# Kernel optimization log

Hardware: AMD Instinct MI355X
Metric: run time of the kernel (lower is better)

## Reference

```python
import jax, jax.numpy as jnp
import numpy as np

EPS_ENERGY = 1e-05
EPS_NORM = 1e-05
DN = ('NWC', 'WIO', 'NWC')  # conv1d dimension numbers: (B,L,C) x (K,Cin,Cout)


def setup_inputs() -> dict:
    key = jax.random.key(0)
    k1, k2 = jax.random.split(key)
    B, L, C = 16, 32768, 21
    K, F = 9, 128
    inputs = jax.random.normal(k1, (B, L, C), dtype=jnp.float32)
    kernel = jax.random.normal(k2, (K, C, F), dtype=jnp.float32)
    # UnitNorm constraint over axes [0, 1] (per output filter)
    kernel = kernel / jnp.sqrt(jnp.sum(kernel * kernel, axis=(0, 1), keepdims=True))
    scale = jnp.full((1, 1, 1), 10.0, dtype=jnp.float32)  # initial_scale
    bias = jnp.zeros((F,), dtype=jnp.float32)
    return {"inputs": inputs, "kernel": kernel, "scale": scale, "bias": bias}


def reference(inputs, kernel, scale, bias):
    # dot: (B, L-K+1, F)
    dot = jax.lax.conv_general_dilated(
        inputs, kernel, window_strides=(1,), padding='VALID',
        dimension_numbers=DN)
    # patch energy: sliding sum of squares over window and ALL input channels.
    # Original convolves sq_inputs with an all-ones (K, C, F) kernel, producing
    # the identical value in every filter channel; we compute it once with a
    # (K, C, 1) ones kernel and broadcast -- same math, less traffic.
    K, C, _ = kernel.shape
    ones_k = jnp.ones((K, C, 1), dtype=inputs.dtype)
    patch_energy = jax.lax.conv_general_dilated(
        inputs * inputs, ones_k, window_strides=(1,), padding='VALID',
        dimension_numbers=DN)  # (B, Lout, 1)
    patch_norms = jnp.sqrt(patch_energy + EPS_ENERGY)
    return scale * (dot / (patch_norms + EPS_NORM)) + bias
```

## Files before the change

### kernel.cpp

```cpp
#include <hip/hip_runtime.h>
#include <hip/hip_bf16.h>
#include <math.h>

typedef __bf16 bf16x8 __attribute__((ext_vector_type(8)));
typedef float  f32x4  __attribute__((ext_vector_type(4)));
typedef unsigned short u16x8 __attribute__((ext_vector_type(8)));

#define B_      16
#define LIN_    32768
#define LOUT_   32760
#define CIN_    21
#define CPAD_   24
#define KT_     9
#define F_      128
#define KSTEPS_ 7
#define TILE_L_ 128
#define ROWS_   136
#define ROWSA_  138
#define NTILE_  256
#define LPAD_   32768
#define IB_ROWS_ 1024
#define IB_PER_B 32
#define WP_OFF_FLOATS_ (B_ * LPAD_)
#define WP_SHORTS_ (4 * KSTEPS_ * 2 * 4 * 16 * 8)

__device__ __forceinline__ unsigned short f2bf(float f) {
  unsigned u = __float_as_uint(f);
  u += 0x7FFFu + ((u >> 16) & 1u);
  return (unsigned short)(u >> 16);
}

__global__ __launch_bounds__(256)
void ckn1d_prep(const float* __restrict__ X, const float* __restrict__ W,
                const float* __restrict__ scale_p, float* __restrict__ ws)
{
  const int tid = threadIdx.x;
  const int bid = blockIdx.x;

  if (bid < B_ * IB_PER_B) {
    __shared__ float rowsq[IB_ROWS_ + 8];
    const int b    = bid >> 5;
    const int base = (bid & (IB_PER_B - 1)) * IB_ROWS_;
    const float scale = scale_p[0];
    const float* Xb = X + (size_t)b * LIN_ * CIN_;

    for (int r = tid; r < IB_ROWS_ + 8; r += 256) {
      int row = base + r;
      float s = 0.f;
      if (row < LIN_) {
        const float* xr = Xb + (size_t)row * CIN_;
        #pragma unroll
        for (int c = 0; c < CIN_; ++c) { float x = xr[c]; s += x * x; }
      }
      rowsq[r] = s;
    }
    __syncthreads();

    const int l0 = tid * 4;
    float e0 = 0.f;
    #pragma unroll
    for (int t = 0; t < KT_; ++t) e0 += rowsq[l0 + t];
    float e1 = e0 - rowsq[l0]     + rowsq[l0 + KT_];
    float e2 = e1 - rowsq[l0 + 1] + rowsq[l0 + 1 + KT_];
    float e3 = e2 - rowsq[l0 + 2] + rowsq[l0 + 2 + KT_];
    f32x4 iv;
    iv[0] = scale / (sqrtf(e0 + 1e-5f) + 1e-5f);
    iv[1] = scale / (sqrtf(e1 + 1e-5f) + 1e-5f);
    iv[2] = scale / (sqrtf(e2 + 1e-5f) + 1e-5f);
    iv[3] = scale / (sqrtf(e3 + 1e-5f) + 1e-5f);
    float* invp = ws + (size_t)b * LPAD_ + base + l0;
    if (base + l0 + 3 < LOUT_) {
      *(f32x4*)invp = iv;
    } else {
      #pragma unroll
      for (int u = 0; u < 4; ++u)
        if (base + l0 + u < LOUT_) invp[u] = iv[u];
    }
  } else {
    const int wv = bid - B_ * IB_PER_B;
    unsigned short* Wp = (unsigned short*)(ws + WP_OFF_FLOATS_);
    for (int idx = tid; idx < KSTEPS_ * 2 * 4 * 16; idx += 256) {
      int t   = idx >> 7;
      int rem = idx & 127;
      int nf  = rem >> 6;
      int q   = (rem >> 4) & 3;
      int la  = rem & 15;
      u16x8 v;
      #pragma unroll
      for (int j = 0; j < 8; ++j) {
        int r = t * 32 + q * 8 + j;
        int k = r / CPAD_;
        int c = r - k * CPAD_;
        float w = 0.f;
        if (c < CIN_ && k < KT_) w = W[(k * CIN_ + c) * F_ + wv * 32 + nf * 16 + la];
        v[j] = f2bf(w);
      }
      *(u16x8*)&Wp[(size_t)((((wv * KSTEPS_ + t) * 2 + nf) * 4 + q) * 16 + la) * 8] = v;
    }
  }
}

__global__ __launch_bounds__(256, 4)
void ckn1d_main(const float* __restrict__ X, const float* __restrict__ ws,
                const float* __restrict__ bias_p, float* __restrict__ Y)
{
  __shared__ __align__(16) unsigned short tileA[ROWSA_ * CPAD_];

  const int tid  = threadIdx.x;
  const int wv   = tid >> 6;
  const int lane = tid & 63;
  const int la   = lane & 15;
  const int q    = lane >> 4;

  const int bx   = blockIdx.x;
  const int b    = bx >> 8;
  const int tile = bx & (NTILE_ - 1);
  const int l0t  = tile * TILE_L_;

  const int f0 = wv * 32 + la;
  const float bias0 = bias_p[f0];
  const float bias1 = bias_p[f0 + 16];

  const float* __restrict__ Xb   = X + (size_t)b * LIN_ * CIN_;
  const float* __restrict__ invb = ws + (size_t)b * LPAD_ + l0t;
  const unsigned short* __restrict__ Wp = (const unsigned short*)(ws + WP_OFF_FLOATS_);
  float* __restrict__ Yb = Y + (size_t)b * LOUT_ * F_;

  for (int i = tid; i < ROWSA_ * 3; i += 256) {
    int r = i / 3;
    tileA[r * CPAD_ + CIN_ + (i - r * 3)] = 0;
  }
  for (int i = tid; i < 2 * CIN_; i += 256) {
    int r = ROWS_ + i / CIN_;
    tileA[r * CPAD_ + (i % CIN_)] = 0;
  }
  {
    const float4* src4 = (const float4*)(Xb + (size_t)l0t * CIN_);
    const int n4v = (min(ROWS_, LIN_ - l0t) * CIN_) >> 2;
    for (int i4 = tid; i4 < (ROWS_ * CIN_) / 4; i4 += 256) {
      float4 v;
      if (i4 < n4v) v = src4[i4];
      else          v = make_float4(0.f, 0.f, 0.f, 0.f);
      int base = i4 * 4;
      #pragma unroll
      for (int e = 0; e < 4; ++e) {
        int idx = base + e;
        int r = idx / CIN_;
        int c = idx - r * CIN_;
        float x = (e == 0) ? v.x : (e == 1) ? v.y : (e == 2) ? v.z : v.w;
        tileA[r * CPAD_ + c] = f2bf(x);
      }
    }
  }

  u16x8 bw[KSTEPS_][2];
  #pragma unroll
  for (int t = 0; t < KSTEPS_; ++t)
    #pragma unroll
    for (int nf = 0; nf < 2; ++nf)
      bw[t][nf] = *(const u16x8*)&Wp[(size_t)((((wv * KSTEPS_ + t) * 2 + nf) * 4 + q) * 16 + la) * 8];

  __syncthreads();

  const f32x4 fzero = {0.f, 0.f, 0.f, 0.f};
  const bool full = (l0t + TILE_L_) <= LOUT_;

  #pragma unroll 1
  for (int mf = 0; mf < TILE_L_ / 16; ++mf) {
    const unsigned short* arow = &tileA[(mf * 16 + la) * CPAD_ + q * 8];
    f32x4 a0 = fzero, a1 = fzero;
    #pragma unroll
    for (int t = 0; t < KSTEPS_; ++t) {
      bf16x8 a = *(const bf16x8*)&arow[t * 32];
      a0 = __builtin_amdgcn_mfma_f32_16x16x32_bf16(
          a, __builtin_bit_cast(bf16x8, bw[t][0]), a0, 0, 0, 0);
      a1 = __builtin_amdgcn_mfma_f32_16x16x32_bf16(
          a, __builtin_bit_cast(bf16x8, bw[t][1]), a1, 0, 0, 0);
    }
    const int lrow0 = mf * 16 + q * 4;
    const f32x4 iv4 = *(const f32x4*)&invb[lrow0];
    float* yo = Yb + (size_t)(l0t + lrow0) * F_ + f0;
    if (full) {
      #pragma unroll
      for (int rg = 0; rg < 4; ++rg) {
        float iv = iv4[rg];
        yo[(size_t)rg * F_]      = a0[rg] * iv + bias0;
        yo[(size_t)rg * F_ + 16] = a1[rg] * iv + bias1;
      }
    } else {
      #pragma unroll
      for (int rg = 0; rg < 4; ++rg) {
        float iv = iv4[rg];
        if (l0t + lrow0 + rg < LOUT_) {
          yo[(size_t)rg * F_]      = a0[rg] * iv + bias0;
          yo[(size_t)rg * F_ + 16] = a1[rg] * iv + bias1;
        }
      }
    }
  }
}

extern "C" void kernel_launch(void* const* d_in, const int* in_sizes, int n_in,
                              void* d_out, int out_size, void* d_ws, size_t ws_size,
                              hipStream_t stream) {
  const float* X  = (const float*)d_in[0];
  const float* W  = (const float*)d_in[1];
  const float* S  = (const float*)d_in[2];
  const float* Bi = (const float*)d_in[3];
  float* Y  = (float*)d_out;
  float* ws = (float*)d_ws;

  dim3 gprep(B_ * IB_PER_B + 4), block(256);
  ckn1d_prep<<<gprep, block, 0, stream>>>(X, W, S, ws);

  dim3 gmain(B_ * NTILE_);
  ckn1d_main<<<gmain, block, 0, stream>>>(X, ws, Bi, Y);
}
```

Baseline: 76.75 us.

## Fuse patch-energy normalization into main conv kernel using LDS row sums

Moves the per-position sliding sum of squares and inverse-norm computation out of the prep kernel and into the main kernel. Row energies are accumulated with LDS atomics while the input tile is staged, and the inverse norms are kept in shared memory. This removes a second full read of the input, plus the global write and read of the inverse-norm array. In exchange it adds LDS atomics and two extra barriers per block, and the prep kernel now only packs the weights.

Result: slower. 102.2 us (+33.2%).

```diff
diff --git a/kernel.cpp b/kernel.cpp
--- a/kernel.cpp
+++ b/kernel.cpp
@@ -18,10 +18,6 @@
 #define ROWS_   136
 #define ROWSA_  138
 #define NTILE_  256
-#define LPAD_   32768
-#define IB_ROWS_ 1024
-#define IB_PER_B 32
-#define WP_OFF_FLOATS_ (B_ * LPAD_)
 #define WP_SHORTS_ (4 * KSTEPS_ * 2 * 4 * 16 * 8)
 
 __device__ __forceinline__ unsigned short f2bf(float f) {
@@ -30,81 +26,45 @@
   return (unsigned short)(u >> 16);
 }
 
+__device__ __forceinline__ void bar_lds() {
+  asm volatile("s_waitcnt lgkmcnt(0)" ::: "memory");
+  __builtin_amdgcn_s_barrier();
+}
+
 __global__ __launch_bounds__(256)
-void ckn1d_prep(const float* __restrict__ X, const float* __restrict__ W,
-                const float* __restrict__ scale_p, float* __restrict__ ws)
+void ckn1d_prep(const float* __restrict__ W, float* __restrict__ ws)
 {
   const int tid = threadIdx.x;
-  const int bid = blockIdx.x;
-
-  if (bid < B_ * IB_PER_B) {
-    __shared__ float rowsq[IB_ROWS_ + 8];
-    const int b    = bid >> 5;
-    const int base = (bid & (IB_PER_B - 1)) * IB_ROWS_;
-    const float scale = scale_p[0];
-    const float* Xb = X + (size_t)b * LIN_ * CIN_;
-
-    for (int r = tid; r < IB_ROWS_ + 8; r += 256) {
-      int row = base + r;
-      float s = 0.f;
-      if (row < LIN_) {
-        const float* xr = Xb + (size_t)row * CIN_;
-        #pragma unroll
-        for (int c = 0; c < CIN_; ++c) { float x = xr[c]; s += x * x; }
-      }
-      rowsq[r] = s;
+  const int wv  = blockIdx.x;
+  unsigned short* Wp = (unsigned short*)ws;
+  for (int idx = tid; idx < KSTEPS_ * 2 * 4 * 16; idx += 256) {
+    int t   = idx >> 7;
+    int rem = idx & 127;
+    int nf  = rem >> 6;
+    int q   = (rem >> 4) & 3;
+    int la  = rem & 15;
+    u16x8 v;
+    #pragma unroll
+    for (int j = 0; j < 8; ++j) {
+      int r = t * 32 + q * 8 + j;
+      int k = r / CPAD_;
+      int c = r - k * CPAD_;
+      float w = 0.f;
+      if (c < CIN_ && k < KT_) w = W[(k * CIN_ + c) * F_ + wv * 32 + nf * 16 + la];
+      v[j] = f2bf(w);
     }
-    __syncthreads();
-
-    const int l0 = tid * 4;
-    float e0 = 0.f;
-    #pragma unroll
-    for (int t = 0; t < KT_; ++t) e0 += rowsq[l0 + t];
-    float e1 = e0 - rowsq[l0]     + rowsq[l0 + KT_];
-    float e2 = e1 - rowsq[l0 + 1] + rowsq[l0 + 1 + KT_];
-    float e3 = e2 - rowsq[l0 + 2] + rowsq[l0 + 2 + KT_];
-    f32x4 iv;
-    iv[0] = scale / (sqrtf(e0 + 1e-5f) + 1e-5f);
-    iv[1] = scale / (sqrtf(e1 + 1e-5f) + 1e-5f);
-    iv[2] = scale / (sqrtf(e2 + 1e-5f) + 1e-5f);
-    iv[3] = scale / (sqrtf(e3 + 1e-5f) + 1e-5f);
-    float* invp = ws + (size_t)b * LPAD_ + base + l0;
-    if (base + l0 + 3 < LOUT_) {
-      *(f32x4*)invp = iv;
-    } else {
-      #pragma unroll
-      for (int u = 0; u < 4; ++u)
-        if (base + l0 + u < LOUT_) invp[u] = iv[u];
-    }
-  } else {
-    const int wv = bid - B_ * IB_PER_B;
-    unsigned short* Wp = (unsigned short*)(ws + WP_OFF_FLOATS_);
-    for (int idx = tid; idx < KSTEPS_ * 2 * 4 * 16; idx += 256) {
-      int t   = idx >> 7;
-      int rem = idx & 127;
-      int nf  = rem >> 6;
-      int q   = (rem >> 4) & 3;
-      int la  = rem & 15;
-      u16x8 v;
-      #pragma unroll
-      for (int j = 0; j < 8; ++j) {
-        int r = t * 32 + q * 8 + j;
-        int k = r / CPAD_;
-        int c = r - k * CPAD_;
-        float w = 0.f;
-        if (c < CIN_ && k < KT_) w = W[(k * CIN_ + c) * F_ + wv * 32 + nf * 16 + la];
-        v[j] = f2bf(w);
-      }
-      *(u16x8*)&Wp[(size_t)((((wv * KSTEPS_ + t) * 2 + nf) * 4 + q) * 16 + la) * 8] = v;
-    }
+    *(u16x8*)&Wp[(size_t)((((wv * KSTEPS_ + t) * 2 + nf) * 4 + q) * 16 + la) * 8] = v;
   }
 }
 
 __global__ __launch_bounds__(256, 4)
 void ckn1d_main(const float* __restrict__ X, const float* __restrict__ ws,
-                const float* __restrict__ bias_p, float* __restrict__ Y)
+                const float* __restrict__ scale_p, const float* __restrict__ bias_p,
+                float* __restrict__ Y)
 {
   __shared__ __align__(16) unsigned short tileA[ROWSA_ * CPAD_];
+  __shared__ float rowsq[ROWS_];
+  __shared__ __align__(16) float inv_s[TILE_L_];
 
   const int tid  = threadIdx.x;
   const int wv   = tid >> 6;
@@ -118,14 +78,15 @@
   const int l0t  = tile * TILE_L_;
 
   const int f0 = wv * 32 + la;
+  const float scale = scale_p[0];
   const float bias0 = bias_p[f0];
   const float bias1 = bias_p[f0 + 16];
 
-  const float* __restrict__ Xb   = X + (size_t)b * LIN_ * CIN_;
-  const float* __restrict__ invb = ws + (size_t)b * LPAD_ + l0t;
-  const unsigned short* __restrict__ Wp = (const unsigned short*)(ws + WP_OFF_FLOATS_);
+  const float* __restrict__ Xb = X + (size_t)b * LIN_ * CIN_;
+  const unsigned short* __restrict__ Wp = (const unsigned short*)ws;
   float* __restrict__ Yb = Y + (size_t)b * LOUT_ * F_;
 
+  if (tid < ROWS_) rowsq[tid] = 0.f;
   for (int i = tid; i < ROWSA_ * 3; i += 256) {
     int r = i / 3;
     tileA[r * CPAD_ + CIN_ + (i - r * 3)] = 0;
@@ -133,24 +94,6 @@
   for (int i = tid; i < 2 * CIN_; i += 256) {
     int r = ROWS_ + i / CIN_;
     tileA[r * CPAD_ + (i % CIN_)] = 0;
-  }
-  {
-    const float4* src4 = (const float4*)(Xb + (size_t)l0t * CIN_);
-    const int n4v = (min(ROWS_, LIN_ - l0t) * CIN_) >> 2;
-    for (int i4 = tid; i4 < (ROWS_ * CIN_) / 4; i4 += 256) {
-      float4 v;
-      if (i4 < n4v) v = src4[i4];
-      else          v = make_float4(0.f, 0.f, 0.f, 0.f);
-      int base = i4 * 4;
-      #pragma unroll
-      for (int e = 0; e < 4; ++e) {
-        int idx = base + e;
-        int r = idx / CIN_;
-        int c = idx - r * CIN_;
-        float x = (e == 0) ? v.x : (e == 1) ? v.y : (e == 2) ? v.z : v.w;
-        tileA[r * CPAD_ + c] = f2bf(x);
-      }
-    }
   }
 
   u16x8 bw[KSTEPS_][2];
@@ -160,7 +103,40 @@
     for (int nf = 0; nf < 2; ++nf)
       bw[t][nf] = *(const u16x8*)&Wp[(size_t)((((wv * KSTEPS_ + t) * 2 + nf) * 4 + q) * 16 + la) * 8];
 
-  __syncthreads();
+  bar_lds();
+
+  {
+    const float4* src4 = (const float4*)(Xb + (size_t)l0t * CIN_);
+    const int n4v = (min(ROWS_, LIN_ - l0t) * CIN_) >> 2;
+    for (int i4 = tid; i4 < (ROWS_ * CIN_) / 4; i4 += 256) {
+      float4 v;
+      if (i4 < n4v) v = src4[i4];
+      else          v = make_float4(0.f, 0.f, 0.f, 0.f);
+      int base = i4 * 4;
+      int r0 = base / CIN_;
+      float s0 = 0.f, s1 = 0.f;
+      #pragma unroll
+      for (int e = 0; e < 4; ++e) {
+        int idx = base + e;
+        int r = idx / CIN_;
+        int c = idx - r * CIN_;
+        float x = (e == 0) ? v.x : (e == 1) ? v.y : (e == 2) ? v.z : v.w;
+        tileA[r * CPAD_ + c] = f2bf(x);
+        if (r == r0) s0 += x * x; else s1 += x * x;
+      }
+      atomicAdd(&rowsq[r0], s0);
+      if (s1 != 0.f && r0 + 1 < ROWS_) atomicAdd(&rowsq[r0 + 1], s1);
+    }
+  }
+  bar_lds();
+
+  if (tid < TILE_L_) {
+    float e = 0.f;
+    #pragma unroll
+    for (int t = 0; t < KT_; ++t) e += rowsq[tid + t];
+    inv_s[tid] = scale / (sqrtf(e + 1e-5f) + 1e-5f);
+  }
+  bar_lds();
 
   const f32x4 fzero = {0.f, 0.f, 0.f, 0.f};
   const bool full = (l0t + TILE_L_) <= LOUT_;
@@ -178,7 +154,7 @@
           a, __builtin_bit_cast(bf16x8, bw[t][1]), a1, 0, 0, 0);
     }
     const int lrow0 = mf * 16 + q * 4;
-    const f32x4 iv4 = *(const f32x4*)&invb[lrow0];
+    const f32x4 iv4 = *(const f32x4*)&inv_s[lrow0];
     float* yo = Yb + (size_t)(l0t + lrow0) * F_ + f0;
     if (full) {
       #pragma unroll
@@ -210,9 +186,6 @@
   float* Y  = (float*)d_out;
   float* ws = (float*)d_ws;
 
-  dim3 gprep(B_ * IB_PER_B + 4), block(256);
-  ckn1d_prep<<<gprep, block, 0, stream>>>(X, W, S, ws);
-
-  dim3 gmain(B_ * NTILE_);
-  ckn1d_main<<<gmain, block, 0, stream>>>(X, ws, Bi, Y);
+  ckn1d_prep<<<dim3(4), dim3(256), 0, stream>>>(W, ws);
+  ckn1d_main<<<dim3(B_ * NTILE_), dim3(256), 0, stream>>>(X, ws, S, Bi, Y);
 }
```

## Stage output tiles in LDS for coalesced float4 global stores

Applied to the files above, without the earlier changes.

Outputs are now written first to a shared-memory buffer of 32 rows by 128 filters, after two MFMA m-fragments per pass. All 256 threads then write that buffer to global memory as contiguous float4 rows. This replaces the scattered scalar stores, which are strided by 16 floats across lanes, and is meant to improve write coalescing on an output-bandwidth-bound kernel. It adds about 17KB of LDS, which may reduce occupancy, plus extra barriers per pass.

After: 68.96 us, median of 2. 10.1% less time.

```diff
diff --git a/kernel.cpp b/kernel.cpp
--- a/kernel.cpp
+++ b/kernel.cpp
@@ -19,15 +19,20 @@
 #define ROWSA_  138
 #define NTILE_  256
 #define LPAD_   32768
+#define OBST_   136
 #define IB_ROWS_ 1024
 #define IB_PER_B 32
 #define WP_OFF_FLOATS_ (B_ * LPAD_)
-#define WP_SHORTS_ (4 * KSTEPS_ * 2 * 4 * 16 * 8)
 
 __device__ __forceinline__ unsigned short f2bf(float f) {
   unsigned u = __float_as_uint(f);
   u += 0x7FFFu + ((u >> 16) & 1u);
   return (unsigned short)(u >> 16);
+}
+
+__device__ __forceinline__ void bar_lds() {
+  asm volatile("s_waitcnt lgkmcnt(0)" ::: "memory");
+  __builtin_amdgcn_s_barrier();
 }
 
 __global__ __launch_bounds__(256)
@@ -105,6 +110,7 @@
                 const float* __restrict__ bias_p, float* __restrict__ Y)
 {
   __shared__ __align__(16) unsigned short tileA[ROWSA_ * CPAD_];
+  __shared__ __align__(16) float outbuf[32 * OBST_];
 
   const int tid  = threadIdx.x;
   const int wv   = tid >> 6;
@@ -160,40 +166,54 @@
     for (int nf = 0; nf < 2; ++nf)
       bw[t][nf] = *(const u16x8*)&Wp[(size_t)((((wv * KSTEPS_ + t) * 2 + nf) * 4 + q) * 16 + la) * 8];
 
-  __syncthreads();
+  bar_lds();
 
   const f32x4 fzero = {0.f, 0.f, 0.f, 0.f};
-  const bool full = (l0t + TILE_L_) <= LOUT_;
 
   #pragma unroll 1
-  for (int mf = 0; mf < TILE_L_ / 16; ++mf) {
-    const unsigned short* arow = &tileA[(mf * 16 + la) * CPAD_ + q * 8];
-    f32x4 a0 = fzero, a1 = fzero;
-    #pragma unroll
-    for (int t = 0; t < KSTEPS_; ++t) {
-      bf16x8 a = *(const bf16x8*)&arow[t * 32];
-      a0 = __builtin_amdgcn_mfma_f32_16x16x32_bf16(
-          a, __builtin_bit_cast(bf16x8, bw[t][0]), a0, 0, 0, 0);
-      a1 = __builtin_amdgcn_mfma_f32_16x16x32_bf16(
-          a, __builtin_bit_cast(bf16x8, bw[t][1]), a1, 0, 0, 0);
-    }
-    const int lrow0 = mf * 16 + q * 4;
-    const f32x4 iv4 = *(const f32x4*)&invb[lrow0];
-    float* yo = Yb + (size_t)(l0t + lrow0) * F_ + f0;
-    if (full) {
+  for (int mp = 0; mp < 4; ++mp) {
+    f32x4 acc[2][2];
+    #pragma unroll
+    for (int mfl = 0; mfl < 2; ++mfl) {
+      const int mf = mp * 2 + mfl;
+      acc[mfl][0] = fzero; acc[mfl][1] = fzero;
+      const unsigned short* arow = &tileA[(mf * 16 + la) * CPAD_ + q * 8];
+      #pragma unroll
+      for (int t = 0; t < KSTEPS_; ++t) {
+        bf16x8 a = *(const bf16x8*)&arow[t * 32];
+        acc[mfl][0] = __builtin_amdgcn_mfma_f32_16x16x32_bf16(
+            a, __builtin_bit_cast(bf16x8, bw[t][0]), acc[mfl][0], 0, 0, 0);
+        acc[mfl][1] = __builtin_amdgcn_mfma_f32_16x16x32_bf16(
+            a, __builtin_bit_cast(bf16x8, bw[t][1]), acc[mfl][1], 0, 0, 0);
+      }
+    }
+
+    if (mp > 0) bar_lds();
+
+    #pragma unroll
+    for (int mfl = 0; mfl < 2; ++mfl) {
+      const int lrow0 = mfl * 16 + q * 4;
+      const f32x4 iv4 = *(const f32x4*)&invb[mp * 32 + lrow0];
       #pragma unroll
       for (int rg = 0; rg < 4; ++rg) {
         float iv = iv4[rg];
-        yo[(size_t)rg * F_]      = a0[rg] * iv + bias0;
-        yo[(size_t)rg * F_ + 16] = a1[rg] * iv + bias1;
-      }
-    } else {
-      #pragma unroll
-      for (int rg = 0; rg < 4; ++rg) {
-        float iv = iv4[rg];
-        if (l0t + lrow0 + rg < LOUT_) {
-          yo[(size_t)rg * F_]      = a0[rg] * iv + bias0;
-          yo[(size_t)rg * F_ + 16] = a1[rg] * iv + bias1;
+        outbuf[(lrow0 + rg) * OBST_ + f0]      = acc[mfl][0][rg] * iv + bias0;
+        outbuf[(lrow0 + rg) * OBST_ + f0 + 16] = acc[mfl][1][rg] * iv + bias1;
+      }
+    }
+    bar_lds();
+
+    {
+      const int lg0 = l0t + mp * 32;
+      #pragma unroll
+      for (int it = 0; it < 4; ++it) {
+        int i  = tid + it * 256;
+        int r  = i >> 5;
+        int c4 = i & 31;
+        int lg = lg0 + r;
+        if (lg < LOUT_) {
+          float4 v = *(const float4*)&outbuf[r * OBST_ + c4 * 4];
+          *(float4*)&Yb[(size_t)lg * F_ + c4 * 4] = v;
         }
       }
     }
```
